# Kernel tuning notes

Measured on AMD Instinct MI355X. Metric: run time of the kernel, lower is better.

Reference implementation:

```python
import jax, jax.numpy as jnp
import numpy as np
from jax import lax


def conv2d(x, w, b):
    # NCHW valid conv, stride 1 (matches torch Conv2d defaults)
    y = lax.conv_general_dilated(x, w, (1, 1), 'VALID',
                                 dimension_numbers=('NCHW', 'OIHW', 'NCHW'))
    return y + b[None, :, None, None]


def maxpool2(x):
    return lax.reduce_window(x, -jnp.inf, lax.max, (1, 1, 2, 2), (1, 1, 2, 2), 'VALID')


def affine_grid(theta, H, W):
    # F.affine_grid(theta, size, align_corners=True): base coords linspace(-1,1)
    xs = jnp.linspace(-1.0, 1.0, W, dtype=theta.dtype)
    ys = jnp.linspace(-1.0, 1.0, H, dtype=theta.dtype)
    gy, gx = jnp.meshgrid(ys, xs, indexing='ij')
    base = jnp.stack([gx, gy, jnp.ones_like(gx)], axis=-1)  # [H,W,3]
    return jnp.einsum('bij,hwj->bhwi', theta, base)  # [B,H,W,2] (x,y)


def grid_sample_bilinear(x, grid):
    # F.grid_sample(x, grid, mode='bilinear', padding_mode='zeros', align_corners=True)
    B, C, H, W = x.shape
    ix = (grid[..., 0] + 1.0) * 0.5 * (W - 1)  # [B,H,W]
    iy = (grid[..., 1] + 1.0) * 0.5 * (H - 1)
    x0 = jnp.floor(ix); y0 = jnp.floor(iy)
    x1 = x0 + 1.0;      y1 = y0 + 1.0

    def gather(yc, xc):
        yi = jnp.clip(yc, 0, H - 1).astype(jnp.int32)
        xi = jnp.clip(xc, 0, W - 1).astype(jnp.int32)
        # per-batch advanced-index gather -> [B,C,Hg,Wg]
        return jax.vmap(lambda img, yy, xx: img[:, yy, xx])(x, yi, xi)

    def valid(yc, xc):
        return ((xc >= 0) & (xc <= W - 1) & (yc >= 0) & (yc <= H - 1)).astype(x.dtype)

    w00 = (x1 - ix) * (y1 - iy)
    w01 = (ix - x0) * (y1 - iy)
    w10 = (x1 - ix) * (iy - y0)
    w11 = (ix - x0) * (iy - y0)
    out = (gather(y0, x0) * (w00 * valid(y0, x0))[:, None]
           + gather(y0, x1) * (w01 * valid(y0, x1))[:, None]
           + gather(y1, x0) * (w10 * valid(y1, x0))[:, None]
           + gather(y1, x1) * (w11 * valid(y1, x1))[:, None])
    return out


def setup_inputs() -> dict:
    key = jax.random.key(0)
    ks = jax.random.split(key, 8)
    B, C, H, W = 128, 3, 224, 224
    LOC_SIZE = 10 * 52 * 52  # 27040, from conv/pool arithmetic on 224x224
    x = jax.random.normal(ks[0], (B, C, H, W), dtype=jnp.float32)
    conv1_w = jax.random.normal(ks[1], (8, C, 7, 7), dtype=jnp.float32) * (1.0 / np.sqrt(C * 49))
    conv1_b = jnp.zeros((8,), dtype=jnp.float32)
    conv2_w = jax.random.normal(ks[2], (10, 8, 5, 5), dtype=jnp.float32) * (1.0 / np.sqrt(8 * 25))
    conv2_b = jnp.zeros((10,), dtype=jnp.float32)
    fc1_w = jax.random.normal(ks[3], (32, LOC_SIZE), dtype=jnp.float32) * (1.0 / np.sqrt(LOC_SIZE))
    fc1_b = jnp.zeros((32,), dtype=jnp.float32)
    fc2_w = jax.random.normal(ks[4], (6, 32), dtype=jnp.float32) * 0.01
    fc2_b = jnp.array([1.0, 0.0, 0.0, 0.0, 1.0, 0.0], dtype=jnp.float32)
    return {"x": x, "conv1_w": conv1_w, "conv1_b": conv1_b,
            "conv2_w": conv2_w, "conv2_b": conv2_b,
            "fc1_w": fc1_w, "fc1_b": fc1_b, "fc2_w": fc2_w, "fc2_b": fc2_b}


def reference(x, conv1_w, conv1_b, conv2_w, conv2_b, fc1_w, fc1_b, fc2_w, fc2_b):
    B, C, H, W = x.shape
    # localization net
    xs = jax.nn.relu(maxpool2(conv2d(x, conv1_w, conv1_b)))
    xs = jax.nn.relu(maxpool2(conv2d(xs, conv2_w, conv2_b)))
    xs = xs.reshape(B, -1)  # [B, 27040]
    h = jax.nn.relu(xs @ fc1_w.T + fc1_b)
    theta = (h @ fc2_w.T + fc2_b).reshape(-1, 2, 3)
    grid = affine_grid(theta, H, W)
    return grid_sample_bilinear(x, grid)
```

## Files before the change

kernel.cpp:

```cpp
#include <hip/hip_runtime.h>
#include <hip/hip_bf16.h>
#include <stdint.h>

typedef __bf16 bf16x8 __attribute__((ext_vector_type(8)));
typedef float f32x4 __attribute__((ext_vector_type(4)));
typedef unsigned long long u64;

union BFrag { uint32_t u[4]; u64 q[2]; bf16x8 v; };
union R16 { uint4 v; u64 q[2]; };

__device__ __forceinline__ void split1(float f, uint32_t& hi, uint32_t& lo) {
  uint32_t b = __float_as_uint(f);
  hi = b >> 16;
  float fl = f - __uint_as_float(b & 0xFFFF0000u);
  lo = __float_as_uint(fl) >> 16;
}

__global__ __launch_bounds__(256) void k0_wprep(
    const float* __restrict__ w1, const float* __restrict__ w2,
    unsigned short* __restrict__ wpHi, unsigned short* __restrict__ wpLo,
    unsigned short* __restrict__ wp2Hi, unsigned short* __restrict__ wp2Lo) {
  int id = blockIdx.x * 256 + threadIdx.x;
  if (id < 4096) {
    int j = id & 7, n = (id >> 3) & 15, g = (id >> 7) & 3, jf = id >> 9;
    int o = n & 7, half = n >> 3;
    int ky = jf - half, c = j & 3, kx = 2 * g + (j >> 2);
    float f = 0.f;
    if (c < 3 && kx < 7 && ky >= 0 && ky < 7)
      f = w1[o * 147 + c * 49 + ky * 7 + kx];
    uint32_t h, l;
    split1(f, h, l);
    wpHi[id] = (unsigned short)h;
    wpLo[id] = (unsigned short)l;
  }
  if (id < 5120) {
    int j = id & 7, n = (id >> 3) & 15, g = (id >> 7) & 3;
    int hk = id >> 9;
    int h = hk & 1, ky = hk >> 1;
    int c = 4 * h + (j & 3), kx = 2 * g + (j >> 2);
    float f = 0.f;
    if (n < 10 && kx < 5)
      f = w2[n * 200 + c * 25 + ky * 5 + kx];
    uint32_t hh, ll;
    split1(f, hh, ll);
    wp2Hi[id] = (unsigned short)hh;
    wp2Lo[id] = (unsigned short)ll;
  }
}

__global__ __launch_bounds__(256) void k1_mfma(
    const float* __restrict__ x, const unsigned short* __restrict__ wpHi,
    const unsigned short* __restrict__ wpLo, const float* __restrict__ bias,
    float* __restrict__ out) {
  __shared__ unsigned short sI[38 * 40 * 8];
  const int b = blockIdx.z;
  const int x0 = blockIdx.x * 32;
  const int y0blk = blockIdx.y * 32;
  const int tid = threadIdx.x;
  const int lane = tid & 63, wid = tid >> 6;
  const int n = lane & 15, g = lane >> 4;
  const int xh = wid & 1, yq = wid >> 1;

  BFrag bhi[8], blo[8];
#pragma unroll
  for (int jf = 0; jf < 8; ++jf) {
    uint4 th = *(const uint4*)&wpHi[((jf * 4 + g) * 16 + n) * 8];
    uint4 tl = *(const uint4*)&wpLo[((jf * 4 + g) * 16 + n) * 8];
    bhi[jf].u[0] = th.x; bhi[jf].u[1] = th.y;
    bhi[jf].u[2] = th.z; bhi[jf].u[3] = th.w;
    blo[jf].u[0] = tl.x; blo[jf].u[1] = tl.y;
    blo[jf].u[2] = tl.z; blo[jf].u[3] = tl.w;
  }

  const float* xb = x + (size_t)b * 3 * 50176;
  float pv0[6], pv1[6], pv2[6];
#pragma unroll
  for (int u = 0; u < 6; ++u) {
    int pos = tid + u * 256;
    if (pos < 1520) {
      int row = pos / 40, col = pos % 40;
      int gy = y0blk + row; gy = gy < 223 ? gy : 223;
      int gx = x0 + col;    gx = gx < 223 ? gx : 223;
      const float* p = xb + (size_t)gy * 224 + gx;
      pv0[u] = p[0];
      pv1[u] = p[50176];
      pv2[u] = p[100352];
    }
  }
#pragma unroll
  for (int u = 0; u < 6; ++u) {
    int pos = tid + u * 256;
    if (pos < 1520) {
      uint32_t h0, l0, h1, l1, h2, l2;
      split1(pv0[u], h0, l0);
      split1(pv1[u], h1, l1);
      split1(pv2[u], h2, l2);
      uint4 q;
      q.x = h0 | (h1 << 16);
      q.y = h2;
      q.z = l0 | (l1 << 16);
      q.w = l2;
      *(uint4*)&sI[pos * 8] = q;
    }
  }
  __syncthreads();

  const int y0w = y0blk + yq * 16;
  f32x4 acc[8];
#pragma unroll
  for (int i = 0; i < 8; ++i) acc[i] = (f32x4){0.f, 0.f, 0.f, 0.f};

  const int mg = xh * 16 + n + 2 * g;
  const int rbase = yq * 16;
#pragma unroll
  for (int t = 0; t < 22; ++t) {
    const int s0 = ((rbase + t) * 40 + mg) * 8;
    R16 r0, r1;
    r0.v = *(const uint4*)&sI[s0];
    r1.v = *(const uint4*)&sI[s0 + 8];
    BFrag ah, al;
    ah.q[0] = r0.q[0]; al.q[0] = r0.q[1];
    ah.q[1] = r1.q[0]; al.q[1] = r1.q[1];
#pragma unroll
    for (int i = 0; i < 8; ++i) {
      const int jf = t - 2 * i;
      if (jf >= 0 && jf < 8)
        acc[i] = __builtin_amdgcn_mfma_f32_16x16x32_bf16(ah.v, bhi[jf].v, acc[i], 0, 0, 0);
    }
#pragma unroll
    for (int i = 0; i < 8; ++i) {
      const int jf = t - 2 * i;
      if (jf >= 0 && jf < 8)
        acc[i] = __builtin_amdgcn_mfma_f32_16x16x32_bf16(ah.v, blo[jf].v, acc[i], 0, 0, 0);
    }
#pragma unroll
    for (int i = 0; i < 8; ++i) {
      const int jf = t - 2 * i;
      if (jf >= 0 && jf < 8)
        acc[i] = __builtin_amdgcn_mfma_f32_16x16x32_bf16(al.v, bhi[jf].v, acc[i], 0, 0, 0);
    }
  }

  const int o = n & 7;
  const float bs = bias[o];
  const int px0 = x0 / 2 + xh * 8 + 2 * g;
  const int py0 = y0w / 2;
#pragma unroll
  for (int i = 0; i < 8; ++i) {
    float v0 = fmaxf(acc[i][0], acc[i][1]);
    float v1 = fmaxf(acc[i][2], acc[i][3]);
    float p0 = __shfl_xor(v0, 8, 64);
    float p1 = __shfl_xor(v1, 8, 64);
    const int py = py0 + i;
    if (n < 8 && py < 109) {
      float m0 = fmaxf(v0, p0) + bs;
      float m1 = fmaxf(v1, p1) + bs;
      float* op = out + (((size_t)(b * 109 + py)) * 109 + px0) * 8 + o;
      if (px0 < 109)     op[0] = fmaxf(m0, 0.f);
      if (px0 + 1 < 109) op[8] = fmaxf(m1, 0.f);
    }
  }
}

__global__ __launch_bounds__(256) void k2_mfma(
    const float* __restrict__ in, const unsigned short* __restrict__ wpHi,
    const unsigned short* __restrict__ wpLo, const float* __restrict__ bias,
    float* __restrict__ out) {
  __shared__ unsigned short sI[12 * 40 * 16];
  const int b = blockIdx.z;
  const int bx = blockIdx.x;
  const int px0 = (bx < 3) ? bx * 16 : 36;
  const int py0 = blockIdx.y * 4;
  const int x0c = px0 * 2, y0c = py0 * 2;
  const int tid = threadIdx.x;
  const int lane = tid & 63, wid = tid >> 6;
  const int n = lane & 15, g = lane >> 4;
  const int xh = wid & 1, yw = wid >> 1;

  const float* ib = in + (size_t)b * 109 * 109 * 8;
  float v[2][8];
#pragma unroll
  for (int u = 0; u < 2; ++u) {
    int pos = tid + u * 256;
    if (pos < 480) {
      int row = pos / 40, col = pos % 40;
      int gy = y0c + row;
      int gx = x0c + col; gx = gx < 108 ? gx : 108;
      const float* p = ib + ((size_t)gy * 109 + gx) * 8;
      float4 q0 = *(const float4*)p;
      float4 q1 = *(const float4*)(p + 4);
      v[u][0] = q0.x; v[u][1] = q0.y; v[u][2] = q0.z; v[u][3] = q0.w;
      v[u][4] = q1.x; v[u][5] = q1.y; v[u][6] = q1.z; v[u][7] = q1.w;
    }
  }
#pragma unroll
  for (int u = 0; u < 2; ++u) {
    int pos = tid + u * 256;
    if (pos < 480) {
      uint32_t hh[8], ll[8];
#pragma unroll
      for (int c = 0; c < 8; ++c) split1(v[u][c], hh[c], ll[c]);
      uint4 q0, q1;
      q0.x = hh[0] | (hh[1] << 16); q0.y = hh[2] | (hh[3] << 16);
      q0.z = ll[0] | (ll[1] << 16); q0.w = ll[2] | (ll[3] << 16);
      q1.x = hh[4] | (hh[5] << 16); q1.y = hh[6] | (hh[7] << 16);
      q1.z = ll[4] | (ll[5] << 16); q1.w = ll[6] | (ll[7] << 16);
      *(uint4*)&sI[pos * 16] = q0;
      *(uint4*)&sI[pos * 16 + 8] = q1;
    }
  }
  __syncthreads();

  f32x4 acc[4];
#pragma unroll
  for (int i = 0; i < 4; ++i) acc[i] = (f32x4){0.f, 0.f, 0.f, 0.f};

  const int mg = xh * 16 + n + 2 * g;
  const int rbase = yw * 4;
#pragma unroll
  for (int h = 0; h < 2; ++h) {
#pragma unroll
    for (int kyg = 0; kyg < 2; ++kyg) {
      const int ky0 = kyg ? 3 : 0;
      const int nky = kyg ? 2 : 3;
      BFrag bh[3], bl[3];
#pragma unroll
      for (int k = 0; k < 3; ++k) {
        if (k < nky) {
          int idx = ((((ky0 + k) * 2 + h) * 4 + g) * 16 + n) * 8;
          uint4 th = *(const uint4*)&wpHi[idx];
          uint4 tl = *(const uint4*)&wpLo[idx];
          bh[k].u[0] = th.x; bh[k].u[1] = th.y;
          bh[k].u[2] = th.z; bh[k].u[3] = th.w;
          bl[k].u[0] = tl.x; bl[k].u[1] = tl.y;
          bl[k].u[2] = tl.z; bl[k].u[3] = tl.w;
        }
      }
#pragma unroll
      for (int t = 0; t < 8; ++t) {
        const bool anyUse = kyg ? (t >= 3) : (t <= 5);
        if (anyUse) {
          const int s0 = ((rbase + t) * 40 + mg) * 16 + h * 8;
          R16 r0, r1;
          r0.v = *(const uint4*)&sI[s0];
          r1.v = *(const uint4*)&sI[s0 + 16];
          BFrag ah, al;
          ah.q[0] = r0.q[0]; al.q[0] = r0.q[1];
          ah.q[1] = r1.q[0]; al.q[1] = r1.q[1];
#pragma unroll
          for (int k = 0; k < 3; ++k) {
            if (k < nky) {
              const int i = t - (ky0 + k);
              if (i >= 0 && i < 4)
                acc[i] = __builtin_amdgcn_mfma_f32_16x16x32_bf16(ah.v, bh[k].v, acc[i], 0, 0, 0);
            }
          }
#pragma unroll
          for (int k = 0; k < 3; ++k) {
            if (k < nky) {
              const int i = t - (ky0 + k);
              if (i >= 0 && i < 4)
                acc[i] = __builtin_amdgcn_mfma_f32_16x16x32_bf16(ah.v, bl[k].v, acc[i], 0, 0, 0);
            }
          }
#pragma unroll
          for (int k = 0; k < 3; ++k) {
            if (k < nky) {
              const int i = t - (ky0 + k);
              if (i >= 0 && i < 4)
                acc[i] = __builtin_amdgcn_mfma_f32_16x16x32_bf16(al.v, bh[k].v, acc[i], 0, 0, 0);
            }
          }
        }
      }
    }
  }

  if (n < 10) {
    const float bs = bias[n];
    const int pxb = px0 + xh * 8 + 2 * g;
    const int pyb = py0 + yw * 2;
#pragma unroll
    for (int u = 0; u < 2; ++u) {
      f32x4 A0 = acc[2 * u], A1 = acc[2 * u + 1];
      float m0 = fmaxf(fmaxf(A0[0], A0[1]), fmaxf(A1[0], A1[1])) + bs;
      float m1 = fmaxf(fmaxf(A0[2], A0[3]), fmaxf(A1[2], A1[3])) + bs;
      float* op = out + ((size_t)(b * 10 + n) * 52 + pyb + u) * 52 + pxb;
      op[0] = fmaxf(m0, 0.f);
      op[1] = fmaxf(m1, 0.f);
    }
  }
}

__global__ __launch_bounds__(512) void k3_fc1_partial(
    const float* __restrict__ xs, const float* __restrict__ w,
    float* __restrict__ part) {
  __shared__ float sA[2][128 * 64];
  __shared__ float sW[2][64 * 33];
  const int p = blockIdx.x;
  const int tid = threadIdx.x;
  const int half = tid >> 8;
  const int t2 = tid & 255;
  const int n = t2 & 31, bg = t2 >> 5;
  const int k0 = p * 128 + half * 64;

  float acc[16];
#pragma unroll
  for (int i = 0; i < 16; ++i) acc[i] = 0.f;

#pragma unroll
  for (int bb = 0; bb < 4; ++bb) {
    float v[8];
#pragma unroll
    for (int u = 0; u < 8; ++u) {
      int idx = bb * 2048 + u * 256 + t2;
      int bbv = idx >> 6, k = idx & 63;
      int gk = k0 + k;
      v[u] = (gk < 27040) ? xs[bbv * 27040 + gk] : 0.f;
    }
#pragma unroll
    for (int u = 0; u < 8; ++u) {
      int idx = bb * 2048 + u * 256 + t2;
      sA[half][idx] = v[u];
    }
  }
  {
    float v[8];
#pragma unroll
    for (int u = 0; u < 8; ++u) {
      int idx = u * 256 + t2;
      int nn = idx >> 6, k = idx & 63;
      int gk = k0 + k;
      v[u] = (gk < 27040) ? w[nn * 27040 + gk] : 0.f;
    }
#pragma unroll
    for (int u = 0; u < 8; ++u) {
      int idx = u * 256 + t2;
      int nn = idx >> 6, k = idx & 63;
      sW[half][k * 33 + nn] = v[u];
    }
  }
  __syncthreads();

  for (int k = 0; k < 64; k += 4) {
    float w0 = sW[half][(k + 0) * 33 + n];
    float w1 = sW[half][(k + 1) * 33 + n];
    float w2 = sW[half][(k + 2) * 33 + n];
    float w3 = sW[half][(k + 3) * 33 + n];
#pragma unroll
    for (int i = 0; i < 16; ++i) {
      float4 a = *(const float4*)&sA[half][(bg * 16 + i) * 64 + k];
      acc[i] = fmaf(a.x, w0, acc[i]);
      acc[i] = fmaf(a.y, w1, acc[i]);
      acc[i] = fmaf(a.z, w2, acc[i]);
      acc[i] = fmaf(a.w, w3, acc[i]);
    }
  }

  __syncthreads();
  if (half == 1) {
#pragma unroll
    for (int i = 0; i < 16; ++i) sA[0][t2 * 16 + i] = acc[i];
  }
  __syncthreads();
  if (half == 0) {
#pragma unroll
    for (int i = 0; i < 16; ++i) acc[i] += sA[0][t2 * 16 + i];
#pragma unroll
    for (int i = 0; i < 16; ++i)
      part[p * 4096 + (bg * 16 + i) * 32 + n] = acc[i];
  }
}

__global__ __launch_bounds__(256) void k4_reduce(
    const float* __restrict__ part, const float* __restrict__ b1,
    float* __restrict__ h) {
  const int lane = threadIdx.x & 31;
  const int eloc = threadIdx.x >> 5;
  const int e = blockIdx.x * 8 + eloc;
  float s = 0.f;
#pragma unroll
  for (int pc = 0; pc < 8; ++pc) s += part[(pc * 32 + lane) * 4096 + e];
#pragma unroll
  for (int off = 16; off > 0; off >>= 1) s += __shfl_down(s, off, 32);
  if (lane == 0) h[e] = fmaxf(s + b1[e & 31], 0.f);
}

__global__ __launch_bounds__(256) void k5_sample(
    const float* __restrict__ x, const float* __restrict__ h,
    const float* __restrict__ w2, const float* __restrict__ b2,
    float* __restrict__ out) {
  __shared__ float th[6];
  const int b = blockIdx.z;
  if (threadIdx.x < 6) {
    int j = threadIdx.x;
    float s = b2[j];
    for (int m = 0; m < 32; ++m) s = fmaf(h[b * 32 + m], w2[j * 32 + m], s);
    th[j] = s;
  }
  __syncthreads();

  const int pix = blockIdx.x * 256 + threadIdx.x;
  const int hh = pix / 224, ww = pix % 224;
  const float step = 2.0f / 223.0f;
  float gx = ww * step - 1.0f, gy = hh * step - 1.0f;
  float tx = th[0] * gx + th[1] * gy + th[2];
  float ty = th[3] * gx + th[4] * gy + th[5];
  float ix = (tx + 1.0f) * 0.5f * 223.0f;
  float iy = (ty + 1.0f) * 0.5f * 223.0f;
  float x0 = floorf(ix), y0 = floorf(iy);
  float x1 = x0 + 1.f, y1 = y0 + 1.f;
  float wx1 = ix - x0, wx0 = x1 - ix;
  float wy1 = iy - y0, wy0 = y1 - iy;
  float w00 = wx0 * wy0, w01 = wx1 * wy0, w10 = wx0 * wy1, w11 = wx1 * wy1;
  bool vx0 = (x0 >= 0.f) && (x0 <= 223.f);
  bool vx1 = (x1 >= 0.f) && (x1 <= 223.f);
  bool vy0 = (y0 >= 0.f) && (y0 <= 223.f);
  bool vy1 = (y1 >= 0.f) && (y1 <= 223.f);
  w00 = (vx0 && vy0) ? w00 : 0.f;
  w01 = (vx1 && vy0) ? w01 : 0.f;
  w10 = (vx0 && vy1) ? w10 : 0.f;
  w11 = (vx1 && vy1) ? w11 : 0.f;
  int xi0 = (int)fminf(fmaxf(x0, 0.f), 223.f);
  int xi1 = (int)fminf(fmaxf(x1, 0.f), 223.f);
  int yi0 = (int)fminf(fmaxf(y0, 0.f), 223.f);
  int yi1 = (int)fminf(fmaxf(y1, 0.f), 223.f);
#pragma unroll
  for (int c = 0; c < 3; ++c) {
    const float* img = x + (size_t)((b * 3 + c) * 224) * 224;
    float v = img[yi0 * 224 + xi0] * w00 + img[yi0 * 224 + xi1] * w01 +
              img[yi1 * 224 + xi0] * w10 + img[yi1 * 224 + xi1] * w11;
    out[((b * 3 + c) * 224 + hh) * 224 + ww] = v;
  }
}

extern "C" void kernel_launch(void* const* d_in, const int* in_sizes, int n_in,
                              void* d_out, int out_size, void* d_ws,
                              size_t ws_size, hipStream_t stream) {
  const float* x   = (const float*)d_in[0];
  const float* w1  = (const float*)d_in[1];
  const float* b1  = (const float*)d_in[2];
  const float* w2  = (const float*)d_in[3];
  const float* b2  = (const float*)d_in[4];
  const float* fw1 = (const float*)d_in[5];
  const float* fb1 = (const float*)d_in[6];
  const float* fw2 = (const float*)d_in[7];
  const float* fb2 = (const float*)d_in[8];
  float* out = (float*)d_out;

  float* ws   = (float*)d_ws;
  float* out1 = ws;
  float* xs   = out1 + 12166144;
  float* part = xs + 3461120;
  float* hbuf = part + 1048576;
  unsigned short* wpHi  = (unsigned short*)(hbuf + 4096);
  unsigned short* wpLo  = wpHi + 4096;
  unsigned short* wp2Hi = wpLo + 4096;
  unsigned short* wp2Lo = wp2Hi + 5120;

  k0_wprep<<<20, 256, 0, stream>>>(w1, w2, wpHi, wpLo, wp2Hi, wp2Lo);
  k1_mfma<<<dim3(7, 7, 128), 256, 0, stream>>>(x, wpHi, wpLo, b1, out1);
  k2_mfma<<<dim3(4, 13, 128), 256, 0, stream>>>(out1, wp2Hi, wp2Lo, b2, xs);
  k3_fc1_partial<<<256, 512, 0, stream>>>(xs, fw1, part);
  k4_reduce<<<512, 256, 0, stream>>>(part, fb1, hbuf);
  k5_sample<<<dim3(196, 1, 128), 256, 0, stream>>>(x, hbuf, fw2, fb2, out);
}
```

Before: 181.3 us.

## Repack conv2 MFMA K-dimension over channels to cut padded MFMA work

Reorganizes the conv2 bf16x3 MFMA reduction so each 32-wide K slice covers all 8 channels times 4 kx positions, with a separate remainder pass for kx=4 and the last tap. Shared-memory layout stores hi and lo halves contiguously per pixel, and weight packing shrinks from 5120 to 3584 entries. The aim is fewer MFMA issues, since the old scheme padded kx from 5 to 8 and split channels into two halves. The risk lies in the remainder handling, where different lane groups read different rows, and in the weight layout staying consistent with the loads.

```diff
diff --git a/kernel.cpp b/kernel.cpp
--- a/kernel.cpp
+++ b/kernel.cpp
@@ -14,6 +14,13 @@
   hi = b >> 16;
   float fl = f - __uint_as_float(b & 0xFFFF0000u);
   lo = __float_as_uint(fl) >> 16;
+}
+
+__device__ __forceinline__ BFrag ldfrag(const unsigned short* p) {
+  uint4 t = *(const uint4*)p;
+  BFrag f;
+  f.u[0] = t.x; f.u[1] = t.y; f.u[2] = t.z; f.u[3] = t.w;
+  return f;
 }
 
 __global__ __launch_bounds__(256) void k0_wprep(
@@ -33,14 +40,19 @@
     wpHi[id] = (unsigned short)h;
     wpLo[id] = (unsigned short)l;
   }
-  if (id < 5120) {
+  if (id < 3584) {
     int j = id & 7, n = (id >> 3) & 15, g = (id >> 7) & 3;
-    int hk = id >> 9;
-    int h = hk & 1, ky = hk >> 1;
-    int c = 4 * h + (j & 3), kx = 2 * g + (j >> 2);
     float f = 0.f;
-    if (n < 10 && kx < 5)
-      f = w2[n * 200 + c * 25 + ky * 5 + kx];
+    if (n < 10) {
+      if (id < 2560) {
+        int ky = id >> 9;
+        f = w2[n * 200 + j * 25 + ky * 5 + g];
+      } else if (id < 3072) {
+        f = w2[n * 200 + j * 25 + g * 5 + 4];
+      } else {
+        if (g == 3) f = w2[n * 200 + j * 25 + 24];
+      }
+    }
     uint32_t hh, ll;
     split1(f, hh, ll);
     wp2Hi[id] = (unsigned short)hh;
@@ -64,12 +76,8 @@
   BFrag bhi[8], blo[8];
 #pragma unroll
   for (int jf = 0; jf < 8; ++jf) {
-    uint4 th = *(const uint4*)&wpHi[((jf * 4 + g) * 16 + n) * 8];
-    uint4 tl = *(const uint4*)&wpLo[((jf * 4 + g) * 16 + n) * 8];
-    bhi[jf].u[0] = th.x; bhi[jf].u[1] = th.y;
-    bhi[jf].u[2] = th.z; bhi[jf].u[3] = th.w;
-    blo[jf].u[0] = tl.x; blo[jf].u[1] = tl.y;
-    blo[jf].u[2] = tl.z; blo[jf].u[3] = tl.w;
+    bhi[jf] = ldfrag(&wpHi[((jf * 4 + g) * 16 + n) * 8]);
+    blo[jf] = ldfrag(&wpLo[((jf * 4 + g) * 16 + n) * 8]);
   }
 
   const float* xb = x + (size_t)b * 3 * 50176;
@@ -200,13 +208,13 @@
       uint32_t hh[8], ll[8];
 #pragma unroll
       for (int c = 0; c < 8; ++c) split1(v[u][c], hh[c], ll[c]);
-      uint4 q0, q1;
-      q0.x = hh[0] | (hh[1] << 16); q0.y = hh[2] | (hh[3] << 16);
-      q0.z = ll[0] | (ll[1] << 16); q0.w = ll[2] | (ll[3] << 16);
-      q1.x = hh[4] | (hh[5] << 16); q1.y = hh[6] | (hh[7] << 16);
-      q1.z = ll[4] | (ll[5] << 16); q1.w = ll[6] | (ll[7] << 16);
-      *(uint4*)&sI[pos * 16] = q0;
-      *(uint4*)&sI[pos * 16 + 8] = q1;
+      uint4 qh, ql;
+      qh.x = hh[0] | (hh[1] << 16); qh.y = hh[2] | (hh[3] << 16);
+      qh.z = hh[4] | (hh[5] << 16); qh.w = hh[6] | (hh[7] << 16);
+      ql.x = ll[0] | (ll[1] << 16); ql.y = ll[2] | (ll[3] << 16);
+      ql.z = ll[4] | (ll[5] << 16); ql.w = ll[6] | (ll[7] << 16);
+      *(uint4*)&sI[pos * 16] = qh;
+      *(uint4*)&sI[pos * 16 + 8] = ql;
     }
   }
   __syncthreads();
@@ -215,63 +223,80 @@
 #pragma unroll
   for (int i = 0; i < 4; ++i) acc[i] = (f32x4){0.f, 0.f, 0.f, 0.f};
 
-  const int mg = xh * 16 + n + 2 * g;
   const int rbase = yw * 4;
-#pragma unroll
-  for (int h = 0; h < 2; ++h) {
-#pragma unroll
-    for (int kyg = 0; kyg < 2; ++kyg) {
-      const int ky0 = kyg ? 3 : 0;
-      const int nky = kyg ? 2 : 3;
-      BFrag bh[3], bl[3];
-#pragma unroll
-      for (int k = 0; k < 3; ++k) {
-        if (k < nky) {
-          int idx = ((((ky0 + k) * 2 + h) * 4 + g) * 16 + n) * 8;
-          uint4 th = *(const uint4*)&wpHi[idx];
-          uint4 tl = *(const uint4*)&wpLo[idx];
-          bh[k].u[0] = th.x; bh[k].u[1] = th.y;
-          bh[k].u[2] = th.z; bh[k].u[3] = th.w;
-          bl[k].u[0] = tl.x; bl[k].u[1] = tl.y;
-          bl[k].u[2] = tl.z; bl[k].u[3] = tl.w;
-        }
-      }
-#pragma unroll
-      for (int t = 0; t < 8; ++t) {
-        const bool anyUse = kyg ? (t >= 3) : (t <= 5);
-        if (anyUse) {
-          const int s0 = ((rbase + t) * 40 + mg) * 16 + h * 8;
-          R16 r0, r1;
-          r0.v = *(const uint4*)&sI[s0];
-          r1.v = *(const uint4*)&sI[s0 + 16];
-          BFrag ah, al;
-          ah.q[0] = r0.q[0]; al.q[0] = r0.q[1];
-          ah.q[1] = r1.q[0]; al.q[1] = r1.q[1];
-#pragma unroll
-          for (int k = 0; k < 3; ++k) {
-            if (k < nky) {
-              const int i = t - (ky0 + k);
-              if (i >= 0 && i < 4)
-                acc[i] = __builtin_amdgcn_mfma_f32_16x16x32_bf16(ah.v, bh[k].v, acc[i], 0, 0, 0);
-            }
-          }
-#pragma unroll
-          for (int k = 0; k < 3; ++k) {
-            if (k < nky) {
-              const int i = t - (ky0 + k);
-              if (i >= 0 && i < 4)
-                acc[i] = __builtin_amdgcn_mfma_f32_16x16x32_bf16(ah.v, bl[k].v, acc[i], 0, 0, 0);
-            }
-          }
-#pragma unroll
-          for (int k = 0; k < 3; ++k) {
-            if (k < nky) {
-              const int i = t - (ky0 + k);
-              if (i >= 0 && i < 4)
-                acc[i] = __builtin_amdgcn_mfma_f32_16x16x32_bf16(al.v, bh[k].v, acc[i], 0, 0, 0);
-            }
-          }
-        }
+  const int colA = xh * 16 + n + g;
+  const int colR = xh * 16 + n + 4;
+
+  {
+    BFrag bmh[5], bml[5];
+#pragma unroll
+    for (int ky = 0; ky < 5; ++ky) {
+      int idx = ky * 512 + g * 128 + n * 8;
+      bmh[ky] = ldfrag(&wpHi[idx]);
+      bml[ky] = ldfrag(&wpLo[idx]);
+    }
+#pragma unroll
+    for (int t = 0; t < 8; ++t) {
+      const int s0 = ((rbase + t) * 40 + colA) * 16;
+      BFrag ah, al;
+      {
+        R16 rh, rl;
+        rh.v = *(const uint4*)&sI[s0];
+        rl.v = *(const uint4*)&sI[s0 + 8];
+        ah.q[0] = rh.q[0]; ah.q[1] = rh.q[1];
+        al.q[0] = rl.q[0]; al.q[1] = rl.q[1];
+      }
+#pragma unroll
+      for (int ky = 0; ky < 5; ++ky) {
+        const int i = t - ky;
+        if (i >= 0 && i < 4)
+          acc[i] = __builtin_amdgcn_mfma_f32_16x16x32_bf16(ah.v, bmh[ky].v, acc[i], 0, 0, 0);
+      }
+#pragma unroll
+      for (int ky = 0; ky < 5; ++ky) {
+        const int i = t - ky;
+        if (i >= 0 && i < 4)
+          acc[i] = __builtin_amdgcn_mfma_f32_16x16x32_bf16(ah.v, bml[ky].v, acc[i], 0, 0, 0);
+      }
+#pragma unroll
+      for (int ky = 0; ky < 5; ++ky) {
+        const int i = t - ky;
+        if (i >= 0 && i < 4)
+          acc[i] = __builtin_amdgcn_mfma_f32_16x16x32_bf16(al.v, bmh[ky].v, acc[i], 0, 0, 0);
+      }
+    }
+  }
+
+  {
+    BFrag r1h = ldfrag(&wpHi[2560 + g * 128 + n * 8]);
+    BFrag r1l = ldfrag(&wpLo[2560 + g * 128 + n * 8]);
+    BFrag r2h = ldfrag(&wpHi[3072 + g * 128 + n * 8]);
+    BFrag r2l = ldfrag(&wpLo[3072 + g * 128 + n * 8]);
+#pragma unroll
+    for (int i = 0; i < 4; ++i) {
+      {
+        const int s1 = ((rbase + i + g) * 40 + colR) * 16;
+        R16 rh, rl;
+        rh.v = *(const uint4*)&sI[s1];
+        rl.v = *(const uint4*)&sI[s1 + 8];
+        BFrag ah, al;
+        ah.q[0] = rh.q[0]; ah.q[1] = rh.q[1];
+        al.q[0] = rl.q[0]; al.q[1] = rl.q[1];
+        acc[i] = __builtin_amdgcn_mfma_f32_16x16x32_bf16(ah.v, r1h.v, acc[i], 0, 0, 0);
+        acc[i] = __builtin_amdgcn_mfma_f32_16x16x32_bf16(ah.v, r1l.v, acc[i], 0, 0, 0);
+        acc[i] = __builtin_amdgcn_mfma_f32_16x16x32_bf16(al.v, r1h.v, acc[i], 0, 0, 0);
+      }
+      {
+        const int s2 = ((rbase + i + 1 + g) * 40 + colR) * 16;
+        R16 rh, rl;
+        rh.v = *(const uint4*)&sI[s2];
+        rl.v = *(const uint4*)&sI[s2 + 8];
+        BFrag ah, al;
+        ah.q[0] = rh.q[0]; ah.q[1] = rh.q[1];
+        al.q[0] = rl.q[0]; al.q[1] = rl.q[1];
+        acc[i] = __builtin_amdgcn_mfma_f32_16x16x32_bf16(ah.v, r2h.v, acc[i], 0, 0, 0);
+        acc[i] = __builtin_amdgcn_mfma_f32_16x16x32_bf16(ah.v, r2l.v, acc[i], 0, 0, 0);
+        acc[i] = __builtin_amdgcn_mfma_f32_16x16x32_bf16(al.v, r2h.v, acc[i], 0, 0, 0);
       }
     }
   }
@@ -456,7 +481,7 @@
   unsigned short* wpHi  = (unsigned short*)(hbuf + 4096);
   unsigned short* wpLo  = wpHi + 4096;
   unsigned short* wp2Hi = wpLo + 4096;
-  unsigned short* wp2Lo = wp2Hi + 5120;
+  unsigned short* wp2Lo = wp2Hi + 4096;
 
   k0_wprep<<<20, 256, 0, stream>>>(w1, w2, wpHi, wpLo, wp2Hi, wp2Lo);
   k1_mfma<<<dim3(7, 7, 128), 256, 0, stream>>>(x, wpHi, wpLo, b1, out1);
```

New measurement: 174.7 us, median of 2. 3.7% less time.
